# Kernel tuning notes

Measured on AMD Instinct MI355X. Metric: run time of the kernel, lower is better.

The kernel has to match this reference:

```python
import jax, jax.numpy as jnp
import numpy as np

FEATS = [13, 26, 52]
NUM_CLASSES = 20
# 9 anchor wh scales (large->small so anchors 0-2 map to the 13x13 layer), normalized by 416
ANC_SCALES = np.array([[116, 90], [156, 198], [373, 326],
                       [30, 61], [62, 45], [59, 119],
                       [10, 13], [16, 30], [33, 23]], dtype=np.float32) / 416.0
LAYER_OFFSETS = np.array([0.0, 13 * 13 * 3, 13 * 13 * 3 + 26 * 26 * 3], dtype=np.float32)


def _build_anchor_tables():
    ancs, fsz = [], []
    for li, f in enumerate(FEATS):
        ys, xs = np.meshgrid(np.arange(f), np.arange(f), indexing='ij')
        # cell top-left corner (col/f, row/f), row-major cell order (row*f+col)
        xy = (np.stack([xs, ys], -1).reshape(-1, 2).astype(np.float32)) / f
        xy3 = np.repeat(xy, 3, axis=0)
        wh3 = np.tile(ANC_SCALES[li * 3:(li + 1) * 3], (f * f, 1))
        ancs.append(np.concatenate([xy3, wh3], -1))
        fsz.append(np.full((f * f * 3, 2), f, dtype=np.float32))
    return np.concatenate(ancs, 0), np.concatenate(fsz, 0)


def _xywh2ltrb(b):
    return jnp.concatenate([b[..., :2] - b[..., 2:] / 2, b[..., :2] + b[..., 2:] / 2], -1)


def _focal(logits, y, alpha=0.25, gamma=2.0):
    bce = jnp.clip(logits, 0.0) - logits * y + jnp.log1p(jnp.exp(-jnp.abs(logits)))
    p = jax.nn.sigmoid(logits)
    pt = y * p + (1.0 - y) * (1.0 - p)
    af = y * alpha + (1.0 - y) * (1.0 - alpha)
    return jnp.sum(bce * af * (1.0 - pt) ** gamma)


def _ciou_pairwise(a, b):
    # a: [n,4] ltrb, b: [m,4] ltrb -> [n,m] CIoU
    eps = 1e-7
    lt = jnp.maximum(a[:, None, :2], b[None, :, :2])
    rb = jnp.minimum(a[:, None, 2:], b[None, :, 2:])
    wh = jnp.clip(rb - lt, 0.0)
    inter = wh[..., 0] * wh[..., 1]
    wa, ha = a[:, 2] - a[:, 0], a[:, 3] - a[:, 1]
    wb, hb = b[:, 2] - b[:, 0], b[:, 3] - b[:, 1]
    union = (wa * ha)[:, None] + (wb * hb)[None, :] - inter
    iou = inter / (union + eps)
    clt = jnp.minimum(a[:, None, :2], b[None, :, :2])
    crb = jnp.maximum(a[:, None, 2:], b[None, :, 2:])
    cwh = crb - clt
    c2 = cwh[..., 0] ** 2 + cwh[..., 1] ** 2 + eps
    ca = (a[:, :2] + a[:, 2:]) / 2
    cb = (b[:, :2] + b[:, 2:]) / 2
    rho2 = jnp.sum((ca[:, None, :] - cb[None, :, :]) ** 2, -1)
    v = (4.0 / (np.pi ** 2)) * (jnp.arctan(wa / (ha + eps))[:, None]
                                - jnp.arctan(wb / (hb + eps))[None, :]) ** 2
    alpha_t = v / (1.0 - iou + v + eps)
    return iou - rho2 / c2 - alpha_t * v


def _iou_one(a, b):
    # elementwise IoU, a,b: [n,4] ltrb
    eps = 1e-7
    lt = jnp.maximum(a[:, :2], b[:, :2])
    rb = jnp.minimum(a[:, 2:], b[:, 2:])
    wh = jnp.clip(rb - lt, 0.0)
    inter = wh[:, 0] * wh[:, 1]
    area_a = (a[:, 2] - a[:, 0]) * (a[:, 3] - a[:, 1])
    area_b = (b[:, 2] - b[:, 0]) * (b[:, 3] - b[:, 1])
    return inter / (area_a + area_b - inter + eps)


def _per_image(p, gb_ltrb, glabels, ancs, fsize_p_anc):
    # p: [10647, 25]; gb_ltrb: [nb,4]; glabels: [nb]
    feats = jnp.asarray([[13.0, 13.0], [26.0, 26.0], [52.0, 52.0]], p.dtype)
    lay_off = jnp.asarray(LAYER_OFFSETS)
    nb = gb_ltrb.shape[0]
    g_xywh = jnp.concatenate([(gb_ltrb[:, :2] + gb_ltrb[:, 2:]) / 2,
                              gb_ltrb[:, 2:] - gb_ltrb[:, :2]], -1)
    fsize9 = jnp.repeat(feats, 3, axis=0)                      # [9,2]
    colrow = jnp.floor(g_xywh[:, None, :2] * fsize9[None])     # [nb,9,2]
    anc_xy = colrow / fsize9                                   # [nb,9,2]
    anc_wh = jnp.broadcast_to(jnp.asarray(ANC_SCALES)[None], (nb, 9, 2))
    anc_ltrb = _xywh2ltrb(jnp.concatenate([anc_xy, anc_wh], -1)).reshape(nb * 9, 4)
    ids = jnp.arange(nb, dtype=p.dtype)
    iou = _ciou_pairwise(gb_ltrb + ids[:, None], anc_ltrb + jnp.repeat(ids, 9)[:, None])
    max_idx = jnp.argmax(iou, axis=1) % 9                      # best of 9 anchors per box
    layer = max_idx // 3
    crs = colrow[jnp.arange(nb), max_idx]                      # [nb,2] (col,row)
    off_colrow = crs[:, 1] * feats[layer, 0] + crs[:, 0]
    match_pos = (lay_off[layer] + off_colrow * 3.0
                 + (max_idx % 3).astype(p.dtype)).astype(jnp.int32)
    # decode predicted boxes (anc corner + sigmoid offset, exp wh)
    p_xy = jax.nn.sigmoid(p[:, :2]) / fsize_p_anc + ancs[:, :2]
    p_wh = jnp.exp(p[:, 2:4]) * ancs[:, 2:]
    p_ltrb = _xywh2ltrb(jnp.concatenate([p_xy, p_wh], -1))
    # cls loss (positives only)
    t = jax.nn.one_hot(glabels - 1, NUM_CLASSES, dtype=p.dtype)
    l_cls = _focal(p[match_pos, 5:], t) / nb
    # conf loss over all anchors, positives scattered to 1
    gconf = jnp.zeros(p.shape[0], p.dtype).at[match_pos].set(1.0)
    l_conf = _focal(p[:, 4], gconf) / nb
    # box loss on matched anchors
    ious = _iou_one(gb_ltrb, p_ltrb[match_pos])
    w = 2.0 - g_xywh[:, 2] * g_xywh[:, 3]
    l_box = jnp.mean(w * (1.0 - ious))
    return l_cls, l_conf, l_box


def setup_inputs() -> dict:
    key = jax.random.key(0)
    k1, k2, k3, k4 = jax.random.split(key, 4)
    B, NB = 128, 8
    p = jax.random.normal(k1, (B, 10647, 4 + 1 + NUM_CLASSES), jnp.float32)
    cxy = jax.random.uniform(k2, (B, NB, 2), minval=0.15, maxval=0.85)
    wh = jax.random.uniform(k3, (B, NB, 2), minval=0.05, maxval=0.25)
    gboxes = jnp.concatenate([cxy - wh / 2, cxy + wh / 2], -1)
    glabels = jax.random.randint(k4, (B, NB), 1, NUM_CLASSES + 1, jnp.int32)
    ancs_np, fsz_np = _build_anchor_tables()
    return {"p_yolo_ts": p, "gboxes_ltrb": gboxes, "glabels": glabels,
            "ancs": jnp.asarray(ancs_np), "fsize_p_anc": jnp.asarray(fsz_np)}


def reference(p_yolo_ts, gboxes_ltrb, glabels, ancs, fsize_p_anc):
    l_cls, l_conf, l_box = jax.vmap(_per_image, in_axes=(0, 0, 0, None, None))(
        p_yolo_ts, gboxes_ltrb, glabels, ancs, fsize_p_anc)
    w_box, w_conf, w_cls = 1.0, 1.0, 1.0  # cfg.LOSS_WEIGHT
    return jnp.mean(l_box) * w_box + jnp.mean(l_conf) * w_conf + jnp.mean(l_cls) * w_cls
```

## Files before the change

### kernel.cpp

```cpp
#include <hip/hip_runtime.h>
#include <cstdint>
#include <cmath>

#define NA   10647
#define NBOX 8
#define NCLS 20
#define FEPS 1e-7f

__device__ __constant__ float ANC[9][2] = {
    {116.0f/416.0f,  90.0f/416.0f},
    {156.0f/416.0f, 198.0f/416.0f},
    {373.0f/416.0f, 326.0f/416.0f},
    { 30.0f/416.0f,  61.0f/416.0f},
    { 62.0f/416.0f,  45.0f/416.0f},
    { 59.0f/416.0f, 119.0f/416.0f},
    { 10.0f/416.0f,  13.0f/416.0f},
    { 16.0f/416.0f,  30.0f/416.0f},
    { 33.0f/416.0f,  23.0f/416.0f}};
__device__ __constant__ float FEATS_F[3] = {13.0f, 26.0f, 52.0f};
__device__ __constant__ float LAYOFF_F[3] = {0.0f, 507.0f, 2535.0f};

__device__ __forceinline__ float focal_term(float l, float y) {
    float bce = fmaxf(l, 0.0f) - l * y + log1pf(expf(-fabsf(l)));
    float p   = 1.0f / (1.0f + expf(-l));
    float pt  = y * p + (1.0f - y) * (1.0f - p);
    float af  = y * 0.25f + (1.0f - y) * 0.75f;
    float om  = 1.0f - pt;
    return bce * af * om * om;
}

__device__ __forceinline__ float focal0(float x) {
    float e   = expf(-fabsf(x));
    float bce = fmaxf(x, 0.0f) + log1pf(e);
    float inv = 1.0f / (1.0f + e);
    float p   = (x >= 0.0f) ? inv : e * inv;
    return bce * 0.75f * p * p;
}

__global__ __launch_bounds__(256) void k_main(
    const float* __restrict__ p, const float* __restrict__ gboxes,
    const int* __restrict__ glabels, const float* __restrict__ ancs,
    const float* __restrict__ fsz, float* __restrict__ ws,
    int ntot, int S, int conf_blocks)
{
    const int bid = blockIdx.x;

    if (bid < conf_blocks) {
        const int tid = bid * 256 + threadIdx.x;
        float acc = 0.0f;
        if (tid < S) {
            const int i0 = tid, i1 = tid + S, i2 = tid + 2 * S;
            float x0 = p[(size_t)i0 * 25 + 4];
            float x1 = (i1 < ntot) ? p[(size_t)i1 * 25 + 4] : 0.0f;
            float x2 = (i2 < ntot) ? p[(size_t)i2 * 25 + 4] : 0.0f;
            acc = focal0(x0);
            if (i1 < ntot) acc += focal0(x1);
            if (i2 < ntot) acc += focal0(x2);
        }
        for (int off = 32; off; off >>= 1) acc += __shfl_down(acc, off);
        __shared__ float sred[4];
        if ((threadIdx.x & 63) == 0) sred[threadIdx.x >> 6] = acc;
        __syncthreads();
        if (threadIdx.x == 0)
            ws[bid] = sred[0] + sred[1] + sred[2] + sred[3];
        return;
    }

    const int b = bid - conf_blocks;
    const int l = threadIdx.x;

    __shared__ float s_g[NBOX][9];
    __shared__ float s_anc[NBOX][9][4];
    __shared__ float s_cr[NBOX][9][2];
    __shared__ float s_atanA[9];
    __shared__ int   s_match[NBOX];

    if (l < NBOX) {
        const float* gb = gboxes + (size_t)(b * NBOX + l) * 4;
        float gl = gb[0], gt = gb[1], gr = gb[2], gbb = gb[3];
        float cx = (gl + gr) * 0.5f, cy = (gt + gbb) * 0.5f;
        float w = gr - gl, h = gbb - gt;
        s_g[l][0] = gl; s_g[l][1] = gt; s_g[l][2] = gr; s_g[l][3] = gbb;
        s_g[l][4] = cx; s_g[l][5] = cy; s_g[l][6] = w;  s_g[l][7] = h;
        s_g[l][8] = atanf(w / (h + FEPS));
    }
    if (l >= 64 && l < 64 + 9) s_atanA[l - 64] = atanf(ANC[l - 64][0] / (ANC[l - 64][1] + FEPS));
    if (l >= 128 && l < 128 + NBOX * 9) {
        int pair = l - 128;
        int j = pair / 9, k = pair % 9;
        const float* gb = gboxes + (size_t)(b * NBOX + j) * 4;
        float cx = (gb[0] + gb[2]) * 0.5f, cy = (gb[1] + gb[3]) * 0.5f;
        float fs = FEATS_F[k / 3];
        float col = floorf(cx * fs), row = floorf(cy * fs);
        float ax = col / fs, ay = row / fs;
        float aw = ANC[k][0], ah = ANC[k][1];
        s_anc[j][k][0] = ax - aw * 0.5f;
        s_anc[j][k][1] = ay - ah * 0.5f;
        s_anc[j][k][2] = ax + aw * 0.5f;
        s_anc[j][k][3] = ay + ah * 0.5f;
        s_cr[j][k][0] = col; s_cr[j][k][1] = row;
    }
    __syncthreads();

    if (l < 64) {
        const int i = l >> 3, j = l & 7;
        const float fi = (float)i, fj = (float)j;
        float al = s_g[i][0] + fi, at = s_g[i][1] + fi;
        float ar = s_g[i][2] + fi, ab = s_g[i][3] + fi;
        float wa = ar - al, ha = ab - at;
        float cax = (al + ar) * 0.5f, cay = (at + ab) * 0.5f;
        float atg = s_g[i][8];

        float bestv = -1e30f; int besti = 1 << 30;
        #pragma unroll
        for (int k = 0; k < 9; ++k) {
            float bl = s_anc[j][k][0] + fj, bt = s_anc[j][k][1] + fj;
            float br = s_anc[j][k][2] + fj, bb = s_anc[j][k][3] + fj;
            float wb = br - bl, hb = bb - bt;
            float ix = fmaxf(fminf(ar, br) - fmaxf(al, bl), 0.0f);
            float iy = fmaxf(fminf(ab, bb) - fmaxf(at, bt), 0.0f);
            float inter = ix * iy;
            float uni = wa * ha + wb * hb - inter;
            float iou = inter / (uni + FEPS);
            float cw = fmaxf(ar, br) - fminf(al, bl);
            float ch = fmaxf(ab, bb) - fminf(at, bt);
            float c2 = cw * cw + ch * ch + FEPS;
            float cbx = (bl + br) * 0.5f, cby = (bt + bb) * 0.5f;
            float dx = cax - cbx, dy = cay - cby;
            float rho2 = dx * dx + dy * dy;
            float dat = atg - s_atanA[k];
            float v = 0.4052847345693511f * dat * dat;
            float alp = v / (1.0f - iou + v + FEPS);
            float ciou = iou - rho2 / c2 - alp * v;
            int flat = j * 9 + k;
            if (ciou > bestv) { bestv = ciou; besti = flat; }
        }
        for (int off = 4; off; off >>= 1) {
            float ov = __shfl_down(bestv, off, 8);
            int   oi = __shfl_down(besti, off, 8);
            if (ov > bestv || (ov == bestv && oi < besti)) { bestv = ov; besti = oi; }
        }
        if (j == 0) {
            int mk = besti % 9;
            int layer = mk / 3;
            float f = FEATS_F[layer];
            float off_cr = s_cr[i][mk][1] * f + s_cr[i][mk][0];
            s_match[i] = (int)(LAYOFF_F[layer] + off_cr * 3.0f + (float)(mk - layer * 3));
        }
    }
    __syncthreads();

    if (l < 64) {
        const int i = l >> 3, j = l & 7;
        float sum = 0.0f;
        const int m = s_match[i];
        const float* prow = p + ((size_t)b * NA + (size_t)m) * 25;
        const int label = glabels[b * NBOX + i] - 1;
        for (int c = j; c < NCLS; c += 8) {
            float y = (c == label) ? 1.0f : 0.0f;
            sum += focal_term(prow[5 + c], y);
        }
        if (j == 0) {
            bool uniq = true;
            for (int jj = 0; jj < i; ++jj) if (s_match[jj] == m) uniq = false;
            if (uniq) {
                float x = prow[4];
                sum += focal_term(x, 1.0f) - focal0(x);
            }
            float s0 = 1.0f / (1.0f + expf(-prow[0]));
            float s1 = 1.0f / (1.0f + expf(-prow[1]));
            float px = s0 / fsz[2 * m]     + ancs[4 * m];
            float py = s1 / fsz[2 * m + 1] + ancs[4 * m + 1];
            float pw = expf(prow[2]) * ancs[4 * m + 2];
            float ph = expf(prow[3]) * ancs[4 * m + 3];
            float pl = px - pw * 0.5f, pt_ = py - ph * 0.5f;
            float pr = px + pw * 0.5f, pb = py + ph * 0.5f;
            float gl = s_g[i][0], gt = s_g[i][1], gr = s_g[i][2], gbb = s_g[i][3];
            float ix = fmaxf(fminf(gr, pr) - fmaxf(gl, pl), 0.0f);
            float iy = fmaxf(fminf(gbb, pb) - fmaxf(gt, pt_), 0.0f);
            float inter = ix * iy;
            float areaA = (gr - gl) * (gbb - gt);
            float areaB = (pr - pl) * (pb - pt_);
            float iou = inter / (areaA + areaB - inter + FEPS);
            float wbox = 2.0f - s_g[i][6] * s_g[i][7];
            sum += wbox * (1.0f - iou);
        }
        for (int off = 32; off; off >>= 1) sum += __shfl_down(sum, off);
        if (l == 0) ws[conf_blocks + b] = sum;
    }
}

__global__ __launch_bounds__(256) void k_final(const float* __restrict__ ws,
                                               float* __restrict__ out,
                                               int nslots, float scale)
{
    __shared__ float sred[256];
    float acc = 0.0f;
    for (int idx = threadIdx.x; idx < nslots; idx += 256) acc += ws[idx];
    sred[threadIdx.x] = acc;
    __syncthreads();
    for (int s = 128; s > 0; s >>= 1) {
        if (threadIdx.x < s) sred[threadIdx.x] += sred[threadIdx.x + s];
        __syncthreads();
    }
    if (threadIdx.x == 0) out[0] = sred[0] * scale;
}

extern "C" void kernel_launch(void* const* d_in, const int* in_sizes, int n_in,
                              void* d_out, int out_size, void* d_ws, size_t ws_size,
                              hipStream_t stream) {
    const float* p      = (const float*)d_in[0];
    const float* gboxes = (const float*)d_in[1];
    const int*   glab   = (const int*)d_in[2];
    const float* ancs   = (const float*)d_in[3];
    const float* fsz    = (const float*)d_in[4];
    float* out = (float*)d_out;
    float* ws  = (float*)d_ws;

    const int B    = in_sizes[0] / (NA * 25);
    const int ntot = B * NA;
    const int S    = (ntot + 2) / 3;
    const int CB   = (S + 255) / 256;

    hipLaunchKernelGGL(k_main, dim3(CB + B), dim3(256), 0, stream,
                       p, gboxes, glab, ancs, fsz, ws, ntot, S, CB);
    hipLaunchKernelGGL(k_final, dim3(1), dim3(256), 0, stream,
                       ws, out, CB + B, 1.0f / (float)(NBOX * B));
}
```

Measured before the change: 33.62 us.

## Stream full prediction tensor as coalesced float4 loads for conf focal sum

```diff
diff --git a/kernel.cpp b/kernel.cpp
--- a/kernel.cpp
+++ b/kernel.cpp
@@ -6,6 +6,8 @@
 #define NBOX 8
 #define NCLS 20
 #define FEPS 1e-7f
+#define CONF_BLOCKS 2048
+#define T 256
 
 __device__ __constant__ float ANC[9][2] = {
     {116.0f/416.0f,  90.0f/416.0f},
@@ -37,25 +39,41 @@
     return bce * 0.75f * p * p;
 }
 
-__global__ __launch_bounds__(256) void k_main(
+__device__ __forceinline__ float pick_conf(const float4& v, unsigned c0) {
+    return (c0 == 4u) ? v.x : (c0 == 3u) ? v.y : (c0 == 2u) ? v.z : v.w;
+}
+
+__global__ __launch_bounds__(T) void k_main(
     const float* __restrict__ p, const float* __restrict__ gboxes,
     const int* __restrict__ glabels, const float* __restrict__ ancs,
-    const float* __restrict__ fsz, float* __restrict__ ws,
-    int ntot, int S, int conf_blocks)
+    const float* __restrict__ fsz, float* __restrict__ ws, long long n4)
 {
     const int bid = blockIdx.x;
 
-    if (bid < conf_blocks) {
-        const int tid = bid * 256 + threadIdx.x;
+    if (bid < CONF_BLOCKS) {
+        const float4* p4 = (const float4*)p;
+        const long long tid = (long long)bid * T + threadIdx.x;
+        const long long nth = (long long)CONF_BLOCKS * T;
+        unsigned c = (unsigned)(((unsigned long long)tid * 4ull) % 25ull);
+        const unsigned d = (unsigned)(((unsigned long long)nth * 4ull) % 25ull);
         float acc = 0.0f;
-        if (tid < S) {
-            const int i0 = tid, i1 = tid + S, i2 = tid + 2 * S;
-            float x0 = p[(size_t)i0 * 25 + 4];
-            float x1 = (i1 < ntot) ? p[(size_t)i1 * 25 + 4] : 0.0f;
-            float x2 = (i2 < ntot) ? p[(size_t)i2 * 25 + 4] : 0.0f;
-            acc = focal0(x0);
-            if (i1 < ntot) acc += focal0(x1);
-            if (i2 < ntot) acc += focal0(x2);
+        for (long long q = tid; q < n4; q += 4 * nth) {
+            const long long q0 = q, q1 = q + nth, q2 = q + 2 * nth, q3 = q + 3 * nth;
+            unsigned c0 = c;
+            unsigned c1 = c0 + d; if (c1 >= 25u) c1 -= 25u;
+            unsigned c2 = c1 + d; if (c2 >= 25u) c2 -= 25u;
+            unsigned c3 = c2 + d; if (c3 >= 25u) c3 -= 25u;
+            c = c3 + d; if (c >= 25u) c -= 25u;
+            float4 v0, v1, v2, v3;
+            bool b0 = (q0 < n4), b1 = (q1 < n4), b2 = (q2 < n4), b3 = (q3 < n4);
+            if (b0) v0 = p4[q0];
+            if (b1) v1 = p4[q1];
+            if (b2) v2 = p4[q2];
+            if (b3) v3 = p4[q3];
+            if (b0 && c0 >= 1u && c0 <= 4u) acc += focal0(pick_conf(v0, c0));
+            if (b1 && c1 >= 1u && c1 <= 4u) acc += focal0(pick_conf(v1, c1));
+            if (b2 && c2 >= 1u && c2 <= 4u) acc += focal0(pick_conf(v2, c2));
+            if (b3 && c3 >= 1u && c3 <= 4u) acc += focal0(pick_conf(v3, c3));
         }
         for (int off = 32; off; off >>= 1) acc += __shfl_down(acc, off);
         __shared__ float sred[4];
@@ -66,7 +84,7 @@
         return;
     }
 
-    const int b = bid - conf_blocks;
+    const int b = bid - CONF_BLOCKS;
     const int l = threadIdx.x;
 
     __shared__ float s_g[NBOX][9];
@@ -186,7 +204,7 @@
             sum += wbox * (1.0f - iou);
         }
         for (int off = 32; off; off >>= 1) sum += __shfl_down(sum, off);
-        if (l == 0) ws[conf_blocks + b] = sum;
+        if (l == 0) ws[CONF_BLOCKS + b] = sum;
     }
 }
 
@@ -217,13 +235,11 @@
     float* out = (float*)d_out;
     float* ws  = (float*)d_ws;
 
-    const int B    = in_sizes[0] / (NA * 25);
-    const int ntot = B * NA;
-    const int S    = (ntot + 2) / 3;
-    const int CB   = (S + 255) / 256;
-
-    hipLaunchKernelGGL(k_main, dim3(CB + B), dim3(256), 0, stream,
-                       p, gboxes, glab, ancs, fsz, ws, ntot, S, CB);
+    const int B = in_sizes[0] / (NA * 25);
+    const long long n4 = (long long)in_sizes[0] / 4;
+
+    hipLaunchKernelGGL(k_main, dim3(CONF_BLOCKS + B), dim3(T), 0, stream,
+                       p, gboxes, glab, ancs, fsz, ws, n4);
     hipLaunchKernelGGL(k_final, dim3(1), dim3(256), 0, stream,
-                       ws, out, CB + B, 1.0f / (float)(NBOX * B));
-}
+                       ws, out, CONF_BLOCKS + B, 1.0f / (float)(NBOX * B));
+}
```

Measured after the change: 44.59 us. 1.33x slower.
